# Kernel optimization log

Hardware: AMD Instinct MI355X
Metric: run time of the kernel (lower is better)

Reference implementation:

```python
import jax, jax.numpy as jnp
import numpy as np

HEADS = 8
DIM_HEAD = 64
DIM = 512
CTX_DIM = 512
INNER = HEADS * DIM_HEAD  # 512
EPS = 1e-5


def layernorm(x, g):
    # repo-style LayerNorm: learnable gain g only, no bias, biased variance
    mean = jnp.mean(x, axis=-1, keepdims=True)
    var = jnp.var(x, axis=-1, keepdims=True)
    return (x - mean) * jax.lax.rsqrt(var + EPS) * g


def setup_inputs() -> dict:
    key = jax.random.key(0)
    ks = jax.random.split(key, 8)
    b, n, m = 2, 4096, 4096
    x = jax.random.normal(ks[0], (b, n, DIM), dtype=jnp.float32)
    context = jax.random.normal(ks[1], (b, m, CTX_DIM), dtype=jnp.float32)
    mask = jax.random.bernoulli(ks[2], 0.9, (b, m))  # bool [b, m]
    # parameters
    g_x = jnp.ones((DIM,), dtype=jnp.float32)
    null_kv = jax.random.normal(ks[3], (2, DIM_HEAD), dtype=jnp.float32)
    Wq = jax.random.normal(ks[4], (DIM, INNER), dtype=jnp.float32) * (DIM ** -0.5)
    Wkv = jax.random.normal(ks[5], (CTX_DIM, 2 * INNER), dtype=jnp.float32) * (CTX_DIM ** -0.5)
    Wo = jax.random.normal(ks[6], (INNER, DIM), dtype=jnp.float32) * (INNER ** -0.5)
    g_out = jnp.ones((DIM,), dtype=jnp.float32)
    return {"x": x, "context": context, "mask": mask, "g_x": g_x,
            "null_kv": null_kv, "Wq": Wq, "Wkv": Wkv, "Wo": Wo, "g_out": g_out}


def reference(x, context, mask, g_x, null_kv, Wq, Wkv, Wo, g_out):
    b, n, _ = x.shape
    m = context.shape[1]
    scale = DIM_HEAD ** (-0.5)  # cosine_sim=False

    xn = layernorm(x, g_x)
    ctx = context  # norm_context=False -> Identity

    q = (xn @ Wq).reshape(b, n, HEADS, DIM_HEAD)          # b n h d
    kv = (ctx @ Wkv).reshape(b, m, 2, HEADS, DIM_HEAD)     # b m 2 h d
    k, v = kv[:, :, 0], kv[:, :, 1]                        # b m h d

    # prepend the null kv token (shared across b, h)
    nk = jnp.broadcast_to(null_kv[0], (b, 1, HEADS, DIM_HEAD))
    nv = jnp.broadcast_to(null_kv[1], (b, 1, HEADS, DIM_HEAD))
    k = jnp.concatenate([nk, k], axis=1)                   # b (m+1) h d
    v = jnp.concatenate([nv, v], axis=1)

    s = jnp.sqrt(jnp.float32(scale))
    q = q * s
    k = k * s

    sim = jnp.einsum('bihd,bjhd->bhij', q, k)              # b h n (m+1)
    max_neg = -jnp.finfo(sim.dtype).max
    full_mask = jnp.pad(mask, ((0, 0), (1, 0)), constant_values=True)  # null token visible
    sim = jnp.where(full_mask[:, None, None, :], sim, max_neg)

    attn = jax.nn.softmax(sim.astype(jnp.float32), axis=-1).astype(sim.dtype)
    out = jnp.einsum('bhij,bjhd->bihd', attn, v).reshape(b, n, INNER)
    out = out @ Wo
    return layernorm(out, g_out)
```

## Files before the change

kernel.cpp:

```cpp
#include <hip/hip_runtime.h>
#include <cfloat>

typedef unsigned short u16;
typedef unsigned int u32;
typedef __bf16 v8bf16 __attribute__((ext_vector_type(8)));
typedef float v4f32 __attribute__((ext_vector_type(4)));
typedef float v16f32 __attribute__((ext_vector_type(16)));

#define MPAD 4224
#define QKS 0.42466090f
#define GRPS 1024

__device__ __forceinline__ u16 f2bf(float f) {
  union { float f; u32 u; } v; v.f = f;
  u32 u = v.u;
  u32 r = (u + 0x7FFFu + ((u >> 16) & 1u)) >> 16;
  return (u16)r;
}

__device__ __forceinline__ u32 pkbf(float lo, float hi) {
  union { float f; u32 u; } a, c;
  a.f = lo; c.f = hi;
  return __builtin_amdgcn_perm(c.u, a.u, 0x07060302);
}

__device__ __forceinline__ float asf(u32 u) {
  union { u32 u; float f; } v; v.u = u; return v.f;
}

__device__ __forceinline__ void exppack2(v16f32& sA, v16f32& sB, float& lst,
                                         v8bf16 pf[4]) {
  float rsum = 0.f;
#pragma unroll
  for (int i = 0; i < 16; i++) { float p = __builtin_amdgcn_exp2f(sA[i]); sA[i] = p; rsum += p; }
#pragma unroll
  for (int i = 0; i < 16; i++) { float p = __builtin_amdgcn_exp2f(sB[i]); sB[i] = p; rsum += p; }
  float a2 = rsum, b2 = rsum;
  asm("v_permlane32_swap_b32 %0, %1" : "+v"(a2), "+v"(b2));
  lst += a2 + b2;
#pragma unroll
  for (int kc = 0; kc < 2; kc++) {
    v16f32& s = kc ? sB : sA;
#pragma unroll
    for (int s16 = 0; s16 < 2; s16++) {
      u32 w0 = pkbf(s[s16 * 8 + 0], s[s16 * 8 + 1]);
      u32 w1 = pkbf(s[s16 * 8 + 2], s[s16 * 8 + 3]);
      u32 w2 = pkbf(s[s16 * 8 + 4], s[s16 * 8 + 5]);
      u32 w3 = pkbf(s[s16 * 8 + 6], s[s16 * 8 + 7]);
      asm("v_permlane32_swap_b32 %0, %1" : "+v"(w0), "+v"(w2));
      asm("v_permlane32_swap_b32 %0, %1" : "+v"(w1), "+v"(w3));
      union { u32 u[4]; v8bf16 v; } pu;
      pu.u[0] = w0; pu.u[1] = w1; pu.u[2] = w2; pu.u[3] = w3;
      pf[kc * 2 + s16] = pu.v;
    }
  }
}

__global__ __launch_bounds__(256) void prep_all(
    const void* __restrict__ mask, float* __restrict__ mp,
    const float* __restrict__ Wq, const float* __restrict__ Wkv,
    const float* __restrict__ Wo, u16* __restrict__ WqT,
    u16* __restrict__ WkvT, u16* __restrict__ WoT,
    const float* __restrict__ x, const float* __restrict__ g,
    u16* __restrict__ xn, const float4* __restrict__ ctx, u16* __restrict__ cb,
    const float* __restrict__ nullkv, u16* __restrict__ KVt) {
  int bb = blockIdx.x;
  int tid = threadIdx.x;
  if (bb < 33) {
    __shared__ int sflag;
    if (tid == 0) sflag = 0;
    __syncthreads();
    const unsigned char* mb = (const unsigned char*)mask;
    int loc = 0;
#pragma unroll
    for (int k = 0; k < 32; k++) {
      int i = tid * 32 + k;
      if ((i & 3) && mb[i]) loc = 1;
    }
    if (loc) sflag = 1;
    __syncthreads();
    int isbyte = sflag;
    int i = bb * 256 + tid;
    if (i >= 2 * MPAD) return;
    int b = i / MPAD, p = i - b * MPAD;
    float v;
    if (p == 0) v = 0.f;
    else if (p <= 4096) {
      int j = b * 4096 + (p - 1);
      int on = isbyte ? (((const unsigned char*)mask)[j] != 0)
                      : (((const int*)mask)[j] != 0);
      v = on ? 0.f : -1e38f;
    } else v = -1e38f;
    mp[i] = v;
  } else if (bb < 1057) {
    __shared__ float tile[32][33];
    int t = bb - 33;
    const float* in; u16* out; int N; float scale; int base;
    if (t < 256)      { in = Wq;  out = WqT;  N = 512;  scale = QKS; base = t; }
    else if (t < 768) { in = Wkv; out = WkvT; N = 1024; scale = 1.f; base = t - 256; }
    else              { in = Wo;  out = WoT;  N = 512;  scale = 1.f; base = t - 768; }
    const int K = 512;
    int ntiles = N >> 5;
    int bx = base % ntiles, by = base / ntiles;
    int n0 = bx * 32, k0 = by * 32;
    int c = tid & 31, r8 = tid >> 5;
#pragma unroll
    for (int i = 0; i < 4; i++) {
      int r = r8 + i * 8;
      tile[r][c] = in[(size_t)(k0 + r) * N + n0 + c];
    }
    __syncthreads();
#pragma unroll
    for (int i = 0; i < 4; i++) {
      int r = r8 + i * 8;
      out[(size_t)(n0 + r) * K + k0 + c] = f2bf(tile[c][r] * scale);
    }
  } else if (bb < 7201) {
    int local = bb - 1057;
    if (local < 2048) {
      int lane = tid & 63, w = tid >> 6;
      int row = local * 4 + w;
      const float* p = x + (size_t)row * 512 + lane * 8;
      float4 f0 = *(const float4*)p;
      float4 f1 = *(const float4*)(p + 4);
      float v[8] = {f0.x, f0.y, f0.z, f0.w, f1.x, f1.y, f1.z, f1.w};
      float sum = 0.f, sq = 0.f;
#pragma unroll
      for (int i = 0; i < 8; i++) { sum += v[i]; sq += v[i] * v[i]; }
#pragma unroll
      for (int m = 1; m < 64; m <<= 1) { sum += __shfl_xor(sum, m); sq += __shfl_xor(sq, m); }
      float mean = sum * (1.f / 512.f);
      float var = sq * (1.f / 512.f) - mean * mean;
      float rstd = rsqrtf(var + 1e-5f);
      const float* gp = g + lane * 8;
      u16 o[8];
#pragma unroll
      for (int i = 0; i < 8; i++) o[i] = f2bf((v[i] - mean) * rstd * gp[i]);
      *(uint4*)&xn[(size_t)row * 512 + lane * 8] = *(uint4*)o;
    } else {
      int i = (local - 2048) * 256 + tid;
      float4 f = ctx[i];
      u16 o[4] = {f2bf(f.x), f2bf(f.y), f2bf(f.z), f2bf(f.w)};
      *(uint2*)&cb[(size_t)i * 4] = *(uint2*)o;
    }
  } else {
    int bh = bb - 7201;
    size_t tb64 = ((size_t)bh * 66 + 64) * 8192;
    uint4 z = make_uint4(0, 0, 0, 0);
    for (int i = tid; i < 2048; i += 256)
      *(uint4*)&KVt[tb64 + (size_t)i * 8] = z;
    size_t tb0 = (size_t)bh * 66 * 8192;
    if (tid < 64) {
      int d = tid;
      KVt[tb0 + (size_t)(d >> 3) * 512 + (d & 7)] = f2bf(nullkv[d] * QKS);
      KVt[tb0 + 4096 + (size_t)d * 8] = f2bf(nullkv[64 + d]);
    }
  }
}

__device__ __forceinline__ void gemm_core(const u16* __restrict__ A,
    const u16* __restrict__ Bt, u16* __restrict__ outb,
    u16* __restrict__ KVt, int Ncols, int mode, int bidx,
    u16* As , u16* Bs ) {
  int tiles_n = Ncols >> 7;
  int n0 = (bidx % tiles_n) * 128;
  int m0 = (bidx / tiles_n) * 128;
  int tid = threadIdx.x;
  int lane = tid & 63, w = tid >> 6, quad = lane >> 4, l15 = lane & 15;
  int wr = w >> 1, wc = w & 1;
  int srow = tid >> 2, scol = (tid & 3) * 8;
  v4f32 acc[4][4];
#pragma unroll
  for (int i = 0; i < 4; i++)
#pragma unroll
    for (int j = 0; j < 4; j++) acc[i][j] = (v4f32){0.f, 0.f, 0.f, 0.f};

  for (int k0 = 0; k0 < 512; k0 += 32) {
    __syncthreads();
    __builtin_amdgcn_global_load_lds((const u32*)&A[(size_t)(m0 + srow) * 512 + k0 + scol],
                                     (u32*)&As[tid * 8], 16, 0, 0);
    __builtin_amdgcn_global_load_lds((const u32*)&A[(size_t)(m0 + 64 + srow) * 512 + k0 + scol],
                                     (u32*)&As[64 * 32 + tid * 8], 16, 0, 0);
    __builtin_amdgcn_global_load_lds((const u32*)&Bt[(size_t)(n0 + srow) * 512 + k0 + scol],
                                     (u32*)&Bs[tid * 8], 16, 0, 0);
    __builtin_amdgcn_global_load_lds((const u32*)&Bt[(size_t)(n0 + 64 + srow) * 512 + k0 + scol],
                                     (u32*)&Bs[64 * 32 + tid * 8], 16, 0, 0);
    __syncthreads();
    v8bf16 af[4], bf[4];
#pragma unroll
    for (int i = 0; i < 4; i++)
      af[i] = *(const v8bf16*)&As[(wr * 64 + i * 16 + l15) * 32 + quad * 8];
#pragma unroll
    for (int j = 0; j < 4; j++)
      bf[j] = *(const v8bf16*)&Bs[(wc * 64 + j * 16 + l15) * 32 + quad * 8];
#pragma unroll
    for (int i = 0; i < 4; i++)
#pragma unroll
      for (int j = 0; j < 4; j++)
        acc[i][j] = __builtin_amdgcn_mfma_f32_16x16x32_bf16(af[i], bf[j], acc[i][j], 0, 0, 0);
  }
#pragma unroll
  for (int i = 0; i < 4; i++) {
    int rbase = m0 + wr * 64 + i * 16 + quad * 4;
#pragma unroll
    for (int j = 0; j < 4; j++) {
      int col = n0 + wc * 64 + j * 16 + l15;
#pragma unroll
      for (int r = 0; r < 4; r++) {
        float v = acc[i][j][r];
        int row = rbase + r;
        if (mode == 0) {
          outb[(size_t)row * 512 + col] = f2bf(v);
        } else {
          int b2 = row >> 12, mr = row & 4095;
          int kk = mr + 1, kt = kk >> 6, kl = kk & 63;
          int kvsel = col >> 9, hh = (col >> 6) & 7, d = col & 63;
          size_t tb = ((size_t)(b2 * 8 + hh) * 66 + kt) * 8192;
          if (kvsel == 0) {
            int chunk = (((d >> 4) * 2 + ((d >> 3) & 1)) * 2 + (kl >> 5)) * 32 + (kl & 31);
            KVt[tb + (size_t)chunk * 8 + (d & 7)] = f2bf(v * QKS);
          } else {
            int chunk = (((kl >> 4) * 2 + ((kl >> 3) & 1)) * 2 + (d >> 5)) * 32 + (d & 31);
            KVt[tb + 4096 + (size_t)chunk * 8 + (kl & 7)] = f2bf(v);
          }
        }
      }
    }
  }
}

__global__ __launch_bounds__(256) void gemm_qkv(const u16* __restrict__ xn,
    const u16* __restrict__ WqT, u16* __restrict__ qb,
    const u16* __restrict__ cb, const u16* __restrict__ WkvT,
    u16* __restrict__ KVt) {
  __shared__ __attribute__((aligned(16))) u16 As[128 * 32];
  __shared__ __attribute__((aligned(16))) u16 Bs[128 * 32];
  int bb = blockIdx.x;
  if (bb < 256) gemm_core(xn, WqT, qb, nullptr, 512, 0, bb, As, Bs);
  else          gemm_core(cb, WkvT, nullptr, KVt, 1024, 1, bb - 256, As, Bs);
}

__global__ __launch_bounds__(256, 2) void attn_kernel(const u16* __restrict__ q,
    const u16* __restrict__ KVt, const float* __restrict__ maskbias,
    u32* __restrict__ Opart, float* __restrict__ lbuf) {
  int obid = blockIdx.x;
  int bid = (obid & 7) * 64 + (obid >> 3);
  int qt = bid & 15, bhs = bid >> 4;
  int s_p = bhs & 1, bh = bhs >> 1;
  int b = bh >> 3, hh = bh & 7;
  int tid = threadIdx.x, lane = tid & 63, w = tid >> 6;
  int m31 = lane & 31, h = (lane >> 5) & 1;
  int grp = (bh * 16 + qt) * 4 + w;
  int q0 = qt * 256 + w * 64;

  v8bf16 qf[2][4];
#pragma unroll
  for (int qg = 0; qg < 2; qg++) {
    const u16* qp = q + (size_t)(b * 4096 + q0 + qg * 32 + m31) * 512 + hh * 64 + h * 8;
#pragma unroll
    for (int ks = 0; ks < 4; ks++) qf[qg][ks] = *(const v8bf16*)&qp[ks * 16];
  }

  v16f32 acc[2][2];
#pragma unroll
  for (int qg = 0; qg < 2; qg++)
#pragma unroll
    for (int db = 0; db < 2; db++)
#pragma unroll
      for (int i = 0; i < 16; i++) acc[qg][db][i] = 0.f;
  float l_st[2] = {0.f, 0.f};

  const u16* kvb = KVt + (size_t)bh * 66 * 8192 + (size_t)(h * 64 + m31) * 8;
  const float* mg = maskbias + b * MPAD;
  int kt0 = s_p * 33;

  for (int kt = kt0; kt < kt0 + 33; ++kt) {
    const u16* tb = kvb + (size_t)kt * 8192;
    v8bf16 kf[4][2];
#pragma unroll
    for (int ks = 0; ks < 4; ks++)
#pragma unroll
      for (int kc = 0; kc < 2; kc++)
        kf[ks][kc] = *(const v8bf16*)&tb[ks * 1024 + kc * 256];
    v16f32 bias_s[2];
#pragma unroll
    for (int kc = 0; kc < 2; kc++)
#pragma unroll
      for (int gg = 0; gg < 4; gg++) {
        float4 bv = *(const float4*)&mg[kt * 64 + kc * 32 + gg * 8 + h * 4];
        bias_s[kc][gg * 4 + 0] = bv.x;
        bias_s[kc][gg * 4 + 1] = bv.y;
        bias_s[kc][gg * 4 + 2] = bv.z;
        bias_s[kc][gg * 4 + 3] = bv.w;
      }

    v8bf16 pf[2][4];
    {
      v16f32 s0 = bias_s[0], s1 = bias_s[1];
      __builtin_amdgcn_s_setprio(1);
#pragma unroll
      for (int ks = 0; ks < 4; ks++) {
        s0 = __builtin_amdgcn_mfma_f32_32x32x16_bf16(kf[ks][0], qf[0][ks], s0, 0, 0, 0);
        s1 = __builtin_amdgcn_mfma_f32_32x32x16_bf16(kf[ks][1], qf[0][ks], s1, 0, 0, 0);
      }
      __builtin_amdgcn_s_setprio(0);
      exppack2(s0, s1, l_st[0], pf[0]);
    }
    __builtin_amdgcn_s_setprio(1);
#pragma unroll
    for (int ks = 0; ks < 4; ks++) {
      bias_s[0] = __builtin_amdgcn_mfma_f32_32x32x16_bf16(kf[ks][0], qf[1][ks], bias_s[0], 0, 0, 0);
      bias_s[1] = __builtin_amdgcn_mfma_f32_32x32x16_bf16(kf[ks][1], qf[1][ks], bias_s[1], 0, 0, 0);
    }
    __builtin_amdgcn_s_setprio(0);
    exppack2(bias_s[0], bias_s[1], l_st[1], pf[1]);

    v8bf16 vf[4][2];
#pragma unroll
    for (int jb = 0; jb < 4; jb++)
#pragma unroll
      for (int db = 0; db < 2; db++)
        vf[jb][db] = *(const v8bf16*)&tb[4096 + jb * 1024 + db * 256];

    __builtin_amdgcn_s_setprio(1);
#pragma unroll
    for (int qg = 0; qg < 2; qg++)
#pragma unroll
      for (int jb = 0; jb < 4; jb++)
#pragma unroll
        for (int db = 0; db < 2; db++)
          acc[qg][db] = __builtin_amdgcn_mfma_f32_32x32x16_bf16(vf[jb][db], pf[qg][jb], acc[qg][db], 0, 0, 0);
    __builtin_amdgcn_s_setprio(0);
  }

  size_t ob = (size_t)(s_p * GRPS + grp) * 2048;
#pragma unroll
  for (int qg = 0; qg < 2; qg++)
#pragma unroll
    for (int db = 0; db < 2; db++)
#pragma unroll
      for (int rp = 0; rp < 8; rp++)
        Opart[ob + qg * 1024 + (size_t)(db * 8 + rp) * 64 + lane] =
            pkbf(acc[qg][db][2 * rp], acc[qg][db][2 * rp + 1]);
  if (h == 0) {
    lbuf[(size_t)(s_p * GRPS + grp) * 64 + m31] = l_st[0];
    lbuf[(size_t)(s_p * GRPS + grp) * 64 + 32 + m31] = l_st[1];
  }
}

__global__ __launch_bounds__(256) void tail3(const u32* __restrict__ Opart,
    const float* __restrict__ lbuf, const u16* __restrict__ WoT,
    const float* __restrict__ g, float* __restrict__ out) {
  __shared__ __attribute__((aligned(16))) u16 As[64 * 520];
  __shared__ __attribute__((aligned(16))) u16 Bs[512 * 32];
  int bid = blockIdx.x;
  int tid = threadIdx.x;
  int w4 = tid >> 6, lane = tid & 63;
  int m31 = lane & 31, h = (lane >> 5) & 1;
  int b = bid >> 6, qt = (bid >> 2) & 15, w = bid & 3;
  size_t rowbase = (size_t)b * 4096 + qt * 256 + w * 64;

#pragma unroll
  for (int i = 0; i < 4; i++) {
    int u = i * 4 + w4;
    int hh = u >> 1, qg = u & 1;
    int grp = (b * 8 + hh) * 64 + qt * 4 + w;
    float l0 = lbuf[(size_t)grp * 64 + qg * 32 + m31];
    float l1 = lbuf[(size_t)(GRPS + grp) * 64 + qg * 32 + m31];
    float inv = 1.f / (l0 + l1);
#pragma unroll
    for (int db = 0; db < 2; db++)
#pragma unroll
      for (int rp = 0; rp < 8; rp++) {
        u32 a = Opart[(size_t)grp * 2048 + qg * 1024 + (db * 8 + rp) * 64 + lane];
        u32 c = Opart[(size_t)(GRPS + grp) * 2048 + qg * 1024 + (db * 8 + rp) * 64 + lane];
        float fe = (asf(a << 16) + asf(c << 16)) * inv;
        float fo = (asf(a & 0xFFFF0000u) + asf(c & 0xFFFF0000u)) * inv;
        int reg = 2 * rp;
        int d0 = (reg & 3) + 8 * (reg >> 2) + 4 * h + 32 * db;
        *(u32*)&As[(qg * 32 + m31) * 520 + hh * 64 + d0] = pkbf(fe, fo);
      }
  }

  int quad = lane >> 4, l15 = lane & 15;
  int srow = tid >> 2, scol = (tid & 3) * 8;
  v4f32 acc[32];
#pragma unroll
  for (int j = 0; j < 32; j++) acc[j] = (v4f32){0.f, 0.f, 0.f, 0.f};

  for (int k0 = 0; k0 < 512; k0 += 32) {
    __syncthreads();
#pragma unroll
    for (int v = 0; v < 8; v++)
      __builtin_amdgcn_global_load_lds((const u32*)&WoT[(size_t)(v * 64 + srow) * 512 + k0 + scol],
                                       (u32*)&Bs[(size_t)v * 2048 + tid * 8], 16, 0, 0);
    __syncthreads();
    v8bf16 af = *(const v8bf16*)&As[(w4 * 16 + l15) * 520 + k0 + quad * 8];
#pragma unroll
    for (int j = 0; j < 32; j++) {
      v8bf16 bf = *(const v8bf16*)&Bs[(j * 16 + l15) * 32 + quad * 8];
      acc[j] = __builtin_amdgcn_mfma_f32_16x16x32_bf16(af, bf, acc[j], 0, 0, 0);
    }
  }

  float rs[4] = {0.f, 0.f, 0.f, 0.f}, sq[4] = {0.f, 0.f, 0.f, 0.f};
#pragma unroll
  for (int j = 0; j < 32; j++)
#pragma unroll
    for (int r = 0; r < 4; r++) { float v = acc[j][r]; rs[r] += v; sq[r] += v * v; }
#pragma unroll
  for (int m = 1; m < 16; m <<= 1)
#pragma unroll
    for (int r = 0; r < 4; r++) { rs[r] += __shfl_xor(rs[r], m); sq[r] += __shfl_xor(sq[r], m); }
  float mean[4], rstd[4];
#pragma unroll
  for (int r = 0; r < 4; r++) {
    mean[r] = rs[r] * (1.f / 512.f);
    float var = sq[r] * (1.f / 512.f) - mean[r] * mean[r];
    rstd[r] = rsqrtf(var + 1e-5f);
  }
#pragma unroll
  for (int j = 0; j < 32; j++) {
    float gv = g[j * 16 + l15];
#pragma unroll
    for (int r = 0; r < 4; r++) {
      size_t row = rowbase + w4 * 16 + quad * 4 + r;
      out[row * 512 + j * 16 + l15] = (acc[j][r] - mean[r]) * rstd[r] * gv;
    }
  }
}

extern "C" void kernel_launch(void* const* d_in, const int* in_sizes, int n_in,
                              void* d_out, int out_size, void* d_ws, size_t ws_size,
                              hipStream_t stream) {
  const float* x       = (const float*)d_in[0];
  const float* context = (const float*)d_in[1];
  const void*  mask    = d_in[2];
  const float* g_x     = (const float*)d_in[3];
  const float* null_kv = (const float*)d_in[4];
  const float* Wq      = (const float*)d_in[5];
  const float* Wkv     = (const float*)d_in[6];
  const float* Wo      = (const float*)d_in[7];
  const float* g_out   = (const float*)d_in[8];

  char* w = (char*)d_ws;
  size_t off = 0;
  auto alloc = [&](size_t bytes) { size_t o = off; off = (off + bytes + 255) & ~(size_t)255; return o; };

  u16* WqT    = (u16*)(w + alloc((size_t)512 * 512 * 2));
  u16* WkvT   = (u16*)(w + alloc((size_t)1024 * 512 * 2));
  u16* WoT    = (u16*)(w + alloc((size_t)512 * 512 * 2));
  float* mp   = (float*)(w + alloc((size_t)2 * MPAD * 4));
  u16* KVt    = (u16*)(w + alloc((size_t)16 * 66 * 8192 * 2));
  u16* qb     = (u16*)(w + alloc((size_t)8192 * 512 * 2));
  u16* aO     = (u16*)(w + alloc((size_t)8192 * 512 * 2));
  size_t xn_off = alloc((size_t)8192 * 512 * 2);
  size_t cb_off = alloc((size_t)8192 * 512 * 2);
  float* lbb  = (float*)(w + alloc((size_t)2 * GRPS * 64 * 4));
  u16* xn   = (u16*)(w + xn_off);
  u16* cb   = (u16*)(w + cb_off);
  u32* Opart = (u32*)(w + xn_off);
  (void)aO;

  prep_all<<<7217, 256, 0, stream>>>(mask, mp, Wq, Wkv, Wo, WqT, WkvT, WoT,
                                     x, g_x, xn, (const float4*)context, cb,
                                     null_kv, KVt);

  gemm_qkv<<<768, 256, 0, stream>>>(xn, WqT, qb, cb, WkvT, KVt);

  attn_kernel<<<512, 256, 0, stream>>>(qb, KVt, mp, Opart, lbb);

  tail3<<<128, 256, 0, stream>>>(Opart, lbb, WoT, g_out, (float*)d_out);
}
```

Before: 234.8 us.

## Split tail output-projection blocks into 32-row tiles with 2x2 warp layout

New measurement: 227.7 us. -3.0%, faster.

```diff
diff --git a/kernel.cpp b/kernel.cpp
--- a/kernel.cpp
+++ b/kernel.cpp
@@ -351,19 +351,19 @@
 __global__ __launch_bounds__(256) void tail3(const u32* __restrict__ Opart,
     const float* __restrict__ lbuf, const u16* __restrict__ WoT,
     const float* __restrict__ g, float* __restrict__ out) {
-  __shared__ __attribute__((aligned(16))) u16 As[64 * 520];
+  __shared__ __attribute__((aligned(16))) u16 As[32 * 520];
   __shared__ __attribute__((aligned(16))) u16 Bs[512 * 32];
+  __shared__ float part[2][32][2];
   int bid = blockIdx.x;
   int tid = threadIdx.x;
   int w4 = tid >> 6, lane = tid & 63;
   int m31 = lane & 31, h = (lane >> 5) & 1;
-  int b = bid >> 6, qt = (bid >> 2) & 15, w = bid & 3;
-  size_t rowbase = (size_t)b * 4096 + qt * 256 + w * 64;
-
-#pragma unroll
-  for (int i = 0; i < 4; i++) {
-    int u = i * 4 + w4;
-    int hh = u >> 1, qg = u & 1;
+  int qg = bid & 1, w = (bid >> 1) & 3, qt = (bid >> 3) & 15, b = bid >> 7;
+  size_t rowbase = (size_t)b * 4096 + qt * 256 + w * 64 + qg * 32;
+
+#pragma unroll
+  for (int i = 0; i < 2; i++) {
+    int hh = i * 4 + w4;
     int grp = (b * 8 + hh) * 64 + qt * 4 + w;
     float l0 = lbuf[(size_t)grp * 64 + qg * 32 + m31];
     float l1 = lbuf[(size_t)(GRPS + grp) * 64 + qg * 32 + m31];
@@ -378,15 +378,16 @@
         float fo = (asf(a & 0xFFFF0000u) + asf(c & 0xFFFF0000u)) * inv;
         int reg = 2 * rp;
         int d0 = (reg & 3) + 8 * (reg >> 2) + 4 * h + 32 * db;
-        *(u32*)&As[(qg * 32 + m31) * 520 + hh * 64 + d0] = pkbf(fe, fo);
+        *(u32*)&As[m31 * 520 + hh * 64 + d0] = pkbf(fe, fo);
       }
   }
 
   int quad = lane >> 4, l15 = lane & 15;
+  int rg = w4 & 1, cg = w4 >> 1;
   int srow = tid >> 2, scol = (tid & 3) * 8;
-  v4f32 acc[32];
-#pragma unroll
-  for (int j = 0; j < 32; j++) acc[j] = (v4f32){0.f, 0.f, 0.f, 0.f};
+  v4f32 acc[16];
+#pragma unroll
+  for (int j = 0; j < 16; j++) acc[j] = (v4f32){0.f, 0.f, 0.f, 0.f};
 
   for (int k0 = 0; k0 < 512; k0 += 32) {
     __syncthreads();
@@ -395,37 +396,48 @@
       __builtin_amdgcn_global_load_lds((const u32*)&WoT[(size_t)(v * 64 + srow) * 512 + k0 + scol],
                                        (u32*)&Bs[(size_t)v * 2048 + tid * 8], 16, 0, 0);
     __syncthreads();
-    v8bf16 af = *(const v8bf16*)&As[(w4 * 16 + l15) * 520 + k0 + quad * 8];
-#pragma unroll
-    for (int j = 0; j < 32; j++) {
-      v8bf16 bf = *(const v8bf16*)&Bs[(j * 16 + l15) * 32 + quad * 8];
+    v8bf16 af = *(const v8bf16*)&As[(rg * 16 + l15) * 520 + k0 + quad * 8];
+#pragma unroll
+    for (int j = 0; j < 16; j++) {
+      v8bf16 bf = *(const v8bf16*)&Bs[(cg * 256 + j * 16 + l15) * 32 + quad * 8];
       acc[j] = __builtin_amdgcn_mfma_f32_16x16x32_bf16(af, bf, acc[j], 0, 0, 0);
     }
   }
 
   float rs[4] = {0.f, 0.f, 0.f, 0.f}, sq[4] = {0.f, 0.f, 0.f, 0.f};
 #pragma unroll
-  for (int j = 0; j < 32; j++)
+  for (int j = 0; j < 16; j++)
 #pragma unroll
     for (int r = 0; r < 4; r++) { float v = acc[j][r]; rs[r] += v; sq[r] += v * v; }
 #pragma unroll
   for (int m = 1; m < 16; m <<= 1)
 #pragma unroll
     for (int r = 0; r < 4; r++) { rs[r] += __shfl_xor(rs[r], m); sq[r] += __shfl_xor(sq[r], m); }
+  if (l15 == 0) {
+#pragma unroll
+    for (int r = 0; r < 4; r++) {
+      part[cg][rg * 16 + quad * 4 + r][0] = rs[r];
+      part[cg][rg * 16 + quad * 4 + r][1] = sq[r];
+    }
+  }
+  __syncthreads();
   float mean[4], rstd[4];
 #pragma unroll
   for (int r = 0; r < 4; r++) {
-    mean[r] = rs[r] * (1.f / 512.f);
-    float var = sq[r] * (1.f / 512.f) - mean[r] * mean[r];
+    int rl = rg * 16 + quad * 4 + r;
+    float trs = part[0][rl][0] + part[1][rl][0];
+    float tsq = part[0][rl][1] + part[1][rl][1];
+    mean[r] = trs * (1.f / 512.f);
+    float var = tsq * (1.f / 512.f) - mean[r] * mean[r];
     rstd[r] = rsqrtf(var + 1e-5f);
   }
 #pragma unroll
-  for (int j = 0; j < 32; j++) {
-    float gv = g[j * 16 + l15];
+  for (int j = 0; j < 16; j++) {
+    float gv = g[cg * 256 + j * 16 + l15];
 #pragma unroll
     for (int r = 0; r < 4; r++) {
-      size_t row = rowbase + w4 * 16 + quad * 4 + r;
-      out[row * 512 + j * 16 + l15] = (acc[j][r] - mean[r]) * rstd[r] * gv;
+      size_t row = rowbase + rg * 16 + quad * 4 + r;
+      out[row * 512 + cg * 256 + j * 16 + l15] = (acc[j][r] - mean[r]) * rstd[r] * gv;
     }
   }
 }
@@ -470,5 +482,5 @@
 
   attn_kernel<<<512, 256, 0, stream>>>(qb, KVt, mp, Opart, lbb);
 
-  tail3<<<128, 256, 0, stream>>>(Opart, lbb, WoT, g_out, (float*)d_out);
-}
+  tail3<<<256, 256, 0, stream>>>(Opart, lbb, WoT, g_out, (float*)d_out);
+}
```
